# Kernel tuning notes

Measured on AMD Instinct MI355X. Metric: run time of the kernel, lower is better.

The kernel has to match this reference:

```python
import jax, jax.numpy as jnp
import numpy as np

EPS = 1e-5

def _layernorm(x, w, b):
    mu = jnp.mean(x, axis=-1, keepdims=True)
    var = jnp.mean(jnp.square(x - mu), axis=-1, keepdims=True)
    return (x - mu) * jax.lax.rsqrt(var + EPS) * w + b

def setup_inputs() -> dict:
    key = jax.random.key(0)
    ks = jax.random.split(key, 9)
    N, P_DIM, D = 16384, 3072, 1024
    patches = jax.random.normal(ks[0], (N, P_DIM), dtype=jnp.float32)
    bbox_coords = jax.random.uniform(ks[1], (N, 4), dtype=jnp.float32)
    ln1_w = jnp.ones((P_DIM,), dtype=jnp.float32)
    ln1_b = jnp.zeros((P_DIM,), dtype=jnp.float32)
    W_patch = jax.random.normal(ks[2], (D, P_DIM), dtype=jnp.float32) * (P_DIM ** -0.5)
    class_emb = jax.random.normal(ks[3], (1, 1, D), dtype=jnp.float32)
    W_pos = jax.random.normal(ks[4], (D, 4), dtype=jnp.float32) * 0.5
    b_pos = jax.random.normal(ks[5], (D,), dtype=jnp.float32) * 0.02
    class_pos = jax.random.normal(ks[6], (1, D), dtype=jnp.float32)
    return {"patches": patches, "bbox_coords": bbox_coords, "ln1_w": ln1_w,
            "ln1_b": ln1_b, "W_patch": W_patch, "class_emb": class_emb,
            "W_pos": W_pos, "b_pos": b_pos, "class_pos": class_pos}

def reference(patches, bbox_coords, ln1_w, ln1_b, W_patch, class_emb, W_pos, b_pos, class_pos):
    # Batched equivalent of the per-patch loop: LayerNorm -> Linear (no bias).
    # NOTE: torch code computes patch_norm2 but appends the PRE-norm2 embedding,
    # so norm2 is dead code and omitted here.
    x = _layernorm(patches, ln1_w, ln1_b)                      # [N, patch_dim]
    patch_embeds = jnp.einsum('np,dp->nd', x, W_patch)          # [N, D]
    embeddings = jnp.concatenate([class_emb, patch_embeds[None]], axis=1)  # [1, N+1, D]
    pos = jnp.einsum('nc,dc->nd', bbox_coords, W_pos) + b_pos   # [N, D]
    pos_full = jnp.concatenate([class_pos[None], pos[None]], axis=1)       # [1, N+1, D]
    return embeddings + pos_full
```

## Files before the change

kernel.cpp:

```cpp
#include <hip/hip_runtime.h>

typedef unsigned short u16;
typedef __attribute__((ext_vector_type(8))) short bf16x8;
typedef __attribute__((ext_vector_type(16))) float f32x16;

#define AS1C(p) ((const __attribute__((address_space(1))) void*)(p))
#define AS3(p)  ((__attribute__((address_space(3))) void*)(p))

#define CFENCE() asm volatile("" ::: "memory")

__device__ __forceinline__ u16 f2bf(float f) {
    unsigned u = __float_as_uint(f);
    u += 0x7fffu + ((u >> 16) & 1u);
    return (u16)(u >> 16);
}

__global__ __launch_bounds__(256) void prep_kernel(
    const float* __restrict__ x, const float* __restrict__ w,
    const float* __restrict__ b, const float* __restrict__ Wp,
    const float* __restrict__ ce, const float* __restrict__ cp,
    u16* __restrict__ A, u16* __restrict__ Wb, float* __restrict__ out,
    int N, int D, int K)
{
    const int blk = blockIdx.x;
    const int t = threadIdx.x;

    if (blk < N) {
        const float* xr = x + (size_t)blk * K;
        float4 v[3];
#pragma unroll
        for (int i = 0; i < 3; ++i)
            v[i] = *(const float4*)&xr[(i * 256 + t) * 4];

        float s = 0.f;
#pragma unroll
        for (int i = 0; i < 3; ++i) s += v[i].x + v[i].y + v[i].z + v[i].w;
#pragma unroll
        for (int off = 32; off; off >>= 1) s += __shfl_down(s, off);

        __shared__ float red[8];
        const int wid = t >> 6, lane = t & 63;
        if (lane == 0) red[wid] = s;
        __syncthreads();
        const float mu = (red[0] + red[1] + red[2] + red[3]) * (1.0f / 3072.0f);

        float sq = 0.f;
#pragma unroll
        for (int i = 0; i < 3; ++i) {
            float dx = v[i].x - mu, dy = v[i].y - mu, dz = v[i].z - mu, dw = v[i].w - mu;
            sq += dx * dx + dy * dy + dz * dz + dw * dw;
        }
#pragma unroll
        for (int off = 32; off; off >>= 1) sq += __shfl_down(sq, off);
        if (lane == 0) red[4 + wid] = sq;
        __syncthreads();
        const float var = (red[4] + red[5] + red[6] + red[7]) * (1.0f / 3072.0f);
        const float inv = rsqrtf(var + 1e-5f);

#pragma unroll
        for (int i = 0; i < 3; ++i) {
            const int j = (i * 256 + t) * 4;
            const float4 wv = *(const float4*)&w[j];
            const float4 bv = *(const float4*)&b[j];
            ushort4 o;
            o.x = f2bf((v[i].x - mu) * inv * wv.x + bv.x);
            o.y = f2bf((v[i].y - mu) * inv * wv.y + bv.y);
            o.z = f2bf((v[i].z - mu) * inv * wv.z + bv.z);
            o.w = f2bf((v[i].w - mu) * inv * wv.w + bv.w);
            *(ushort4*)&A[(size_t)blk * K + j] = o;
        }
    } else if (blk < N + D) {
        const int row = blk - N;
        const float* wr = Wp + (size_t)row * K;
#pragma unroll
        for (int i = 0; i < 3; ++i) {
            const int j = (i * 256 + t) * 4;
            const float4 v = *(const float4*)&wr[j];
            ushort4 o;
            o.x = f2bf(v.x); o.y = f2bf(v.y); o.z = f2bf(v.z); o.w = f2bf(v.w);
            *(ushort4*)&Wb[(size_t)row * K + j] = o;
        }
    } else {
#pragma unroll
        for (int i = 0; i < 4; ++i) {
            const int j = i * 256 + t;
            out[j] = ce[j] + cp[j];
        }
    }
}

#define STG_A(BUFOFS, R0, T_) \
    __builtin_amdgcn_global_load_lds(AS1C(aS + (size_t)(R0) * 3072 + (T_) * 64), \
                                     AS3(dA + (BUFOFS) + (R0) * 128), 16, 0, 0)
#define STG_B(BUFOFS, R0, T_) \
    __builtin_amdgcn_global_load_lds(AS1C(bS + (size_t)(R0) * 3072 + (T_) * 64), \
                                     AS3(dB + (BUFOFS) + (R0) * 128), 16, 0, 0)

#define MFMA32(d, a, b) d = __builtin_amdgcn_mfma_f32_32x32x16_bf16(a, b, d, 0, 0, 0)

#define LGKM(N_) asm volatile("s_waitcnt lgkmcnt(" #N_ ")" ::: "memory"); \
                 __builtin_amdgcn_sched_barrier(0)

#define RD6(BUF, CK, A0, A1, B0, B1, A2, A3) \
    A0 = *(const bf16x8*)(L + (BUF) + aRowBase + 0 * 4096 + (CK)); \
    A1 = *(const bf16x8*)(L + (BUF) + aRowBase + 1 * 4096 + (CK)); \
    B0 = *(const bf16x8*)(L + (BUF) + bRowBase + 0 * 4096 + (CK)); \
    B1 = *(const bf16x8*)(L + (BUF) + bRowBase + 1 * 4096 + (CK)); \
    A2 = *(const bf16x8*)(L + (BUF) + aRowBase + 2 * 4096 + (CK)); \
    A3 = *(const bf16x8*)(L + (BUF) + aRowBase + 3 * 4096 + (CK))

#define G0(A0, A1, B0, B1) \
    MFMA32(acc[0][0], A0, B0); MFMA32(acc[1][0], A1, B0); \
    MFMA32(acc[0][1], A0, B1); MFMA32(acc[1][1], A1, B1)
#define G1(A2, A3, B0, B1) \
    MFMA32(acc[2][0], A2, B0); MFMA32(acc[3][0], A3, B0); \
    MFMA32(acc[2][1], A2, B1); MFMA32(acc[3][1], A3, B1)

#define TILE(BUF, STG, WT) do {                                                 \
    bf16x8 xa0, xa1, xb0, xb1, xa2, xa3;                                        \
    bf16x8 ya0, ya1, yb0, yb1, ya2, ya3;                                        \
    RD6(BUF, ck0, xa0, xa1, xb0, xb1, xa2, xa3);                                \
    RD6(BUF, ck1, ya0, ya1, yb0, yb1, ya2, ya3);                                \
    STG;                                                                        \
    __builtin_amdgcn_s_setprio(1);                                              \
    LGKM(8); G0(xa0, xa1, xb0, xb1);                                            \
    LGKM(6); G1(xa2, xa3, xb0, xb1);                                            \
    RD6(BUF, ck2, xa0, xa1, xb0, xb1, xa2, xa3);                                \
    LGKM(8); G0(ya0, ya1, yb0, yb1);                                            \
    LGKM(6); G1(ya2, ya3, yb0, yb1);                                            \
    RD6(BUF, ck3, ya0, ya1, yb0, yb1, ya2, ya3);                                \
    LGKM(8); G0(xa0, xa1, xb0, xb1);                                            \
    LGKM(6); G1(xa2, xa3, xb0, xb1);                                            \
    LGKM(2); G0(ya0, ya1, yb0, yb1);                                            \
    LGKM(0); G1(ya2, ya3, yb0, yb1);                                            \
    __builtin_amdgcn_s_setprio(0);                                              \
    WT;                                                                         \
    __builtin_amdgcn_s_barrier();                                               \
    CFENCE();                                                                   \
} while (0)

#define STG_ALL(OBUF, TN) \
    { STG_B(OBUF, 0, TN); STG_B(OBUF, 64, TN); STG_B(OBUF, 128, TN);            \
      STG_B(OBUF, 192, TN); STG_A(OBUF, 0, TN); STG_A(OBUF, 64, TN);            \
      STG_A(OBUF, 128, TN); STG_A(OBUF, 192, TN); }

#define VMW0() asm volatile("s_waitcnt vmcnt(0)" ::: "memory")

__global__ __launch_bounds__(512, 2) void gemm_256_r14_kernel(
    const u16* __restrict__ A, const u16* __restrict__ W,
    const float* __restrict__ bbox, const float* __restrict__ Wpos,
    const float* __restrict__ bpos, float* __restrict__ out,
    int D)
{
    __shared__ __align__(16) char lds[131072];
    const char* L = (const char*)lds;
    const int K = 3072;
    const int NK = 48;

    const int bid = blockIdx.x;
    const int swb = (bid & 7) * 32 + (bid >> 3);
    const int bx = swb & 3;
    const int by = swb >> 2;
    const int brow = by * 256;
    const int bcol = bx * 256;

    const int t = threadIdx.x;
    const int wid = t >> 6, lane = t & 63;
    const int wm = wid >> 2;
    const int wn = wid & 3;
    const int l31 = lane & 31;
    const int klane16 = (lane >> 5) * 16;
    const int xorb = (lane & 7) << 4;
    const int aRowBase = (wm * 128 + l31) * 128;
    const int bRowBase = 32768 + (wn * 64 + l31) * 128;
    const int ck0 = (0  + klane16) ^ xorb;
    const int ck1 = (32 + klane16) ^ xorb;
    const int ck2 = (64 + klane16) ^ xorb;
    const int ck3 = (96 + klane16) ^ xorb;

    const int srow = t >> 3;
    const int scol = ((t & 7) ^ ((t >> 3) & 7)) * 8;
    const u16* aS = A + (size_t)(brow + srow) * K + scol;
    const u16* bS = W + (size_t)(bcol + srow) * K + scol;
    char* dA = (char*)lds + t * 16;
    char* dB = (char*)lds + 32768 + t * 16;

    f32x16 acc[4][2] = {};

    STG_ALL(0, 0);
    VMW0();
    __builtin_amdgcn_s_barrier();
    CFENCE();

    for (int T = 0; T < NK; T += 2) {
        const bool more = (T + 2) < NK;
        TILE(0, STG_ALL(65536, T + 1), { VMW0(); });
        TILE(65536, { if (more) STG_ALL(0, T + 2); }, { if (more) VMW0(); });
    }

    float* Lf = (float*)lds;
    const int lrofs = (lane >> 5) * 4;
    const int cg = bcol + lane * 4;

    float4 wpv[4];
    float bpv[4];
#pragma unroll
    for (int j = 0; j < 4; ++j) {
        wpv[j] = *(const float4*)&Wpos[(cg + j) * 4];
        bpv[j] = bpos[cg + j];
    }

#pragma unroll
    for (int mb = 0; mb < 4; ++mb) {
        __builtin_amdgcn_s_barrier();
        CFENCE();
#pragma unroll
        for (int nb = 0; nb < 2; ++nb) {
            const int cc = wn * 64 + nb * 32 + l31;
#pragma unroll
            for (int reg = 0; reg < 16; ++reg) {
                const int frow = (reg & 3) + 8 * (reg >> 2) + lrofs;
                Lf[(wm * 32 + frow) * 256 + cc] = acc[mb][nb][reg];
            }
        }
        __builtin_amdgcn_s_barrier();
        CFENCE();
#pragma unroll
        for (int i = 0; i < 8; ++i) {
            const int lrow = wid + 8 * i;
            const int gr = brow + (lrow >> 5) * 128 + mb * 32 + (lrow & 31);
            const float4 v = *(const float4*)&Lf[lrow * 256 + lane * 4];
            const float4 bb = *(const float4*)&bbox[(size_t)gr * 4];
            float4 o;
            o.x = v.x + bpv[0] + bb.x * wpv[0].x + bb.y * wpv[0].y + bb.z * wpv[0].z + bb.w * wpv[0].w;
            o.y = v.y + bpv[1] + bb.x * wpv[1].x + bb.y * wpv[1].y + bb.z * wpv[1].z + bb.w * wpv[1].w;
            o.z = v.z + bpv[2] + bb.x * wpv[2].x + bb.y * wpv[2].y + bb.z * wpv[2].z + bb.w * wpv[2].w;
            o.w = v.w + bpv[3] + bb.x * wpv[3].x + bb.y * wpv[3].y + bb.z * wpv[3].z + bb.w * wpv[3].w;
            *(float4*)&out[(size_t)(gr + 1) * D + cg] = o;
        }
    }
}

extern "C" void kernel_launch(void* const* d_in, const int* in_sizes, int n_in,
                              void* d_out, int out_size, void* d_ws, size_t ws_size,
                              hipStream_t stream)
{
    const float* patches   = (const float*)d_in[0];
    const float* bbox      = (const float*)d_in[1];
    const float* ln1_w     = (const float*)d_in[2];
    const float* ln1_b     = (const float*)d_in[3];
    const float* W_patch   = (const float*)d_in[4];
    const float* class_emb = (const float*)d_in[5];
    const float* W_pos     = (const float*)d_in[6];
    const float* b_pos     = (const float*)d_in[7];
    const float* class_pos = (const float*)d_in[8];
    float* out = (float*)d_out;

    const int N = in_sizes[1] / 4;
    const int K = in_sizes[2];
    const int D = in_sizes[7];

    u16* Abf = (u16*)d_ws;
    u16* Wbf = Abf + (size_t)N * K;

    prep_kernel<<<N + D + 1, 256, 0, stream>>>(patches, ln1_w, ln1_b, W_patch,
                                               class_emb, class_pos, Abf, Wbf, out,
                                               N, D, K);

    const int nblk = (N / 256) * (D / 256);
    gemm_256_r14_kernel<<<nblk, 512, 0, stream>>>(Abf, Wbf, bbox, W_pos, b_pos, out, D);
}
```

Baseline: 159.6 us.

## Use 4 waves per block with 128x128 warp tiles in GEMM

Restructures the GEMM from 8 waves (each computing 128x64) to 4 waves per 256x256 block, each computing a 128x128 sub-tile with a 4x4 accumulator grid. Each wave issues 16 MFMAs per 8 LDS fragment reads instead of 8 per 6, which raises arithmetic intensity per LDS read and halves barrier participants. In exchange it doubles accumulator registers (256 VGPRs for acc), halves the threads issuing global-to-LDS loads (so each does twice as many), and reduces latency hiding from the wave count.

```diff
diff --git a/kernel.cpp b/kernel.cpp
--- a/kernel.cpp
+++ b/kernel.cpp
@@ -101,38 +101,39 @@
 #define LGKM(N_) asm volatile("s_waitcnt lgkmcnt(" #N_ ")" ::: "memory"); \
                  __builtin_amdgcn_sched_barrier(0)
 
-#define RD6(BUF, CK, A0, A1, B0, B1, A2, A3) \
+#define RD8(BUF, CK, A0, A1, A2, A3, B0, B1, B2, B3) \
     A0 = *(const bf16x8*)(L + (BUF) + aRowBase + 0 * 4096 + (CK)); \
     A1 = *(const bf16x8*)(L + (BUF) + aRowBase + 1 * 4096 + (CK)); \
+    A2 = *(const bf16x8*)(L + (BUF) + aRowBase + 2 * 4096 + (CK)); \
+    A3 = *(const bf16x8*)(L + (BUF) + aRowBase + 3 * 4096 + (CK)); \
     B0 = *(const bf16x8*)(L + (BUF) + bRowBase + 0 * 4096 + (CK)); \
     B1 = *(const bf16x8*)(L + (BUF) + bRowBase + 1 * 4096 + (CK)); \
-    A2 = *(const bf16x8*)(L + (BUF) + aRowBase + 2 * 4096 + (CK)); \
-    A3 = *(const bf16x8*)(L + (BUF) + aRowBase + 3 * 4096 + (CK))
-
-#define G0(A0, A1, B0, B1) \
+    B2 = *(const bf16x8*)(L + (BUF) + bRowBase + 2 * 4096 + (CK)); \
+    B3 = *(const bf16x8*)(L + (BUF) + bRowBase + 3 * 4096 + (CK))
+
+#define G16(A0, A1, A2, A3, B0, B1, B2, B3) \
     MFMA32(acc[0][0], A0, B0); MFMA32(acc[1][0], A1, B0); \
-    MFMA32(acc[0][1], A0, B1); MFMA32(acc[1][1], A1, B1)
-#define G1(A2, A3, B0, B1) \
     MFMA32(acc[2][0], A2, B0); MFMA32(acc[3][0], A3, B0); \
-    MFMA32(acc[2][1], A2, B1); MFMA32(acc[3][1], A3, B1)
+    MFMA32(acc[0][1], A0, B1); MFMA32(acc[1][1], A1, B1); \
+    MFMA32(acc[2][1], A2, B1); MFMA32(acc[3][1], A3, B1); \
+    MFMA32(acc[0][2], A0, B2); MFMA32(acc[1][2], A1, B2); \
+    MFMA32(acc[2][2], A2, B2); MFMA32(acc[3][2], A3, B2); \
+    MFMA32(acc[0][3], A0, B3); MFMA32(acc[1][3], A1, B3); \
+    MFMA32(acc[2][3], A2, B3); MFMA32(acc[3][3], A3, B3)
 
 #define TILE(BUF, STG, WT) do {                                                 \
-    bf16x8 xa0, xa1, xb0, xb1, xa2, xa3;                                        \
-    bf16x8 ya0, ya1, yb0, yb1, ya2, ya3;                                        \
-    RD6(BUF, ck0, xa0, xa1, xb0, xb1, xa2, xa3);                                \
-    RD6(BUF, ck1, ya0, ya1, yb0, yb1, ya2, ya3);                                \
+    bf16x8 xa0, xa1, xa2, xa3, xb0, xb1, xb2, xb3;                              \
+    bf16x8 ya0, ya1, ya2, ya3, yb0, yb1, yb2, yb3;                              \
+    RD8(BUF, ck0, xa0, xa1, xa2, xa3, xb0, xb1, xb2, xb3);                      \
+    RD8(BUF, ck1, ya0, ya1, ya2, ya3, yb0, yb1, yb2, yb3);                      \
     STG;                                                                        \
     __builtin_amdgcn_s_setprio(1);                                              \
-    LGKM(8); G0(xa0, xa1, xb0, xb1);                                            \
-    LGKM(6); G1(xa2, xa3, xb0, xb1);                                            \
-    RD6(BUF, ck2, xa0, xa1, xb0, xb1, xa2, xa3);                                \
-    LGKM(8); G0(ya0, ya1, yb0, yb1);                                            \
-    LGKM(6); G1(ya2, ya3, yb0, yb1);                                            \
-    RD6(BUF, ck3, ya0, ya1, yb0, yb1, ya2, ya3);                                \
-    LGKM(8); G0(xa0, xa1, xb0, xb1);                                            \
-    LGKM(6); G1(xa2, xa3, xb0, xb1);                                            \
-    LGKM(2); G0(ya0, ya1, yb0, yb1);                                            \
-    LGKM(0); G1(ya2, ya3, yb0, yb1);                                            \
+    LGKM(8); G16(xa0, xa1, xa2, xa3, xb0, xb1, xb2, xb3);                       \
+    RD8(BUF, ck2, xa0, xa1, xa2, xa3, xb0, xb1, xb2, xb3);                      \
+    LGKM(8); G16(ya0, ya1, ya2, ya3, yb0, yb1, yb2, yb3);                       \
+    RD8(BUF, ck3, ya0, ya1, ya2, ya3, yb0, yb1, yb2, yb3);                      \
+    LGKM(8); G16(xa0, xa1, xa2, xa3, xb0, xb1, xb2, xb3);                       \
+    LGKM(0); G16(ya0, ya1, ya2, ya3, yb0, yb1, yb2, yb3);                       \
     __builtin_amdgcn_s_setprio(0);                                              \
     WT;                                                                         \
     __builtin_amdgcn_s_barrier();                                               \
@@ -140,13 +141,16 @@
 } while (0)
 
 #define STG_ALL(OBUF, TN) \
-    { STG_B(OBUF, 0, TN); STG_B(OBUF, 64, TN); STG_B(OBUF, 128, TN);            \
-      STG_B(OBUF, 192, TN); STG_A(OBUF, 0, TN); STG_A(OBUF, 64, TN);            \
-      STG_A(OBUF, 128, TN); STG_A(OBUF, 192, TN); }
+    { STG_B(OBUF, 0, TN);   STG_B(OBUF, 32, TN);  STG_B(OBUF, 64, TN);          \
+      STG_B(OBUF, 96, TN);  STG_B(OBUF, 128, TN); STG_B(OBUF, 160, TN);         \
+      STG_B(OBUF, 192, TN); STG_B(OBUF, 224, TN);                               \
+      STG_A(OBUF, 0, TN);   STG_A(OBUF, 32, TN);  STG_A(OBUF, 64, TN);          \
+      STG_A(OBUF, 96, TN);  STG_A(OBUF, 128, TN); STG_A(OBUF, 160, TN);         \
+      STG_A(OBUF, 192, TN); STG_A(OBUF, 224, TN); }
 
 #define VMW0() asm volatile("s_waitcnt vmcnt(0)" ::: "memory")
 
-__global__ __launch_bounds__(512, 2) void gemm_256_r14_kernel(
+__global__ __launch_bounds__(256, 1) void gemm_256_r15_kernel(
     const u16* __restrict__ A, const u16* __restrict__ W,
     const float* __restrict__ bbox, const float* __restrict__ Wpos,
     const float* __restrict__ bpos, float* __restrict__ out,
@@ -166,13 +170,13 @@
 
     const int t = threadIdx.x;
     const int wid = t >> 6, lane = t & 63;
-    const int wm = wid >> 2;
-    const int wn = wid & 3;
+    const int wm = wid >> 1;
+    const int wn = wid & 1;
     const int l31 = lane & 31;
     const int klane16 = (lane >> 5) * 16;
     const int xorb = (lane & 7) << 4;
     const int aRowBase = (wm * 128 + l31) * 128;
-    const int bRowBase = 32768 + (wn * 64 + l31) * 128;
+    const int bRowBase = 32768 + (wn * 128 + l31) * 128;
     const int ck0 = (0  + klane16) ^ xorb;
     const int ck1 = (32 + klane16) ^ xorb;
     const int ck2 = (64 + klane16) ^ xorb;
@@ -185,7 +189,7 @@
     char* dA = (char*)lds + t * 16;
     char* dB = (char*)lds + 32768 + t * 16;
 
-    f32x16 acc[4][2] = {};
+    f32x16 acc[4][4] = {};
 
     STG_ALL(0, 0);
     VMW0();
@@ -215,8 +219,8 @@
         __builtin_amdgcn_s_barrier();
         CFENCE();
 #pragma unroll
-        for (int nb = 0; nb < 2; ++nb) {
-            const int cc = wn * 64 + nb * 32 + l31;
+        for (int nb = 0; nb < 4; ++nb) {
+            const int cc = wn * 128 + nb * 32 + l31;
 #pragma unroll
             for (int reg = 0; reg < 16; ++reg) {
                 const int frow = (reg & 3) + 8 * (reg >> 2) + lrofs;
@@ -226,8 +230,8 @@
         __builtin_amdgcn_s_barrier();
         CFENCE();
 #pragma unroll
-        for (int i = 0; i < 8; ++i) {
-            const int lrow = wid + 8 * i;
+        for (int i = 0; i < 16; ++i) {
+            const int lrow = wid + 4 * i;
             const int gr = brow + (lrow >> 5) * 128 + mb * 32 + (lrow & 31);
             const float4 v = *(const float4*)&Lf[lrow * 256 + lane * 4];
             const float4 bb = *(const float4*)&bbox[(size_t)gr * 4];
@@ -268,5 +272,5 @@
                                                N, D, K);
 
     const int nblk = (N / 256) * (D / 256);
-    gemm_256_r14_kernel<<<nblk, 512, 0, stream>>>(Abf, Wbf, bbox, W_pos, b_pos, out, D);
-}
+    gemm_256_r15_kernel<<<nblk, 256, 0, stream>>>(Abf, Wbf, bbox, W_pos, b_pos, out, D);
+}
```

Result: slower. 233.3 us (+46.2%).
